# Performance work log

Measured on AMD Instinct MI355X. Metric: run time of the kernel, lower is better.

Reference implementation:

```python
import jax, jax.numpy as jnp
import numpy as np
from jax import lax

RATIO = 0.25
K = 16
EPS = 1e-5
B, N, CX, COUT, CAUX = 16, 4096, 64, 128, 32


def _fps(p, m):
    # Farthest point sampling on one cloud p:(N,3); deterministic start at index 0.
    mind = jnp.sum((p - p[0]) ** 2, axis=-1)  # (N,) min sq-dist to selected set
    def step(mind, _):
        nxt = jnp.argmax(mind)
        d = jnp.sum((p - p[nxt]) ** 2, axis=-1)
        return jnp.minimum(mind, d), nxt
    _, rest = lax.scan(step, mind, None, length=m - 1)
    return jnp.concatenate([jnp.zeros((1,), jnp.int32), rest.astype(jnp.int32)])


def setup_inputs() -> dict:
    key = jax.random.key(0)
    k1, k2, k3, k4, k5, k6 = jax.random.split(key, 6)
    P = B * N
    x = jax.random.normal(k1, (P, CX), jnp.float32)
    pos = jax.random.normal(k2, (P, 3), jnp.float32)
    batch = jnp.repeat(jnp.arange(B, dtype=jnp.int32), N)  # equal-size clouds
    aux = jax.random.normal(k3, (P, CAUX), jnp.float32)
    # MLP params: Linear(CX->COUT) + BatchNorm affine
    W = jax.random.normal(k4, (CX, COUT), jnp.float32) * (1.0 / np.sqrt(CX))
    b = jax.random.normal(k5, (COUT,), jnp.float32) * 0.02
    gamma = jnp.ones((COUT,), jnp.float32) + 0.1 * jax.random.normal(k6, (COUT,), jnp.float32)
    beta = jnp.zeros((COUT,), jnp.float32)
    return {"x": x, "pos": pos, "batch": batch, "aux": aux,
            "W": W, "b": b, "gamma": gamma, "beta": beta}


def reference(x, pos, batch, aux, W, b, gamma, beta):
    P = x.shape[0]
    nb = int(batch[-1]) + 1            # number of clouds (equal-size)
    n = P // nb
    m = int(n * RATIO)                 # clusters per cloud
    pos_b = pos.reshape(nb, n, 3)
    # --- FPS per cloud ---
    idx_local = jax.vmap(lambda p: _fps(p, m))(pos_b)                     # (B, M)
    id_clusters = (idx_local + jnp.arange(nb, dtype=jnp.int32)[:, None] * n).reshape(-1)
    centers = jnp.take_along_axis(pos_b, idx_local[..., None], axis=1)    # (B, M, 3)
    # --- kNN of all points to cluster centers, within each cloud ---
    d2 = jnp.sum((centers[:, :, None, :] - pos_b[:, None, :, :]) ** 2, axis=-1)  # (B, M, N)
    _, nb_local = lax.top_k(-d2, K)                                       # (B, M, K)
    nb_global = (nb_local + jnp.arange(nb, dtype=jnp.int32)[:, None, None] * n).reshape(-1)
    # --- MLP: Linear -> BatchNorm(batch stats, train mode) -> ReLU ---
    h = x @ W + b
    mu = jnp.mean(h, axis=0)
    var = jnp.var(h, axis=0)
    x_trans = jax.nn.relu(gamma * (h - mu) * lax.rsqrt(var + EPS) + beta)  # (P, Cout)
    # --- gather + per-cluster max / mean pooling (== scatter over knn edges) ---
    x_out = jnp.max(x_trans[nb_global].reshape(nb * m, K, -1), axis=1)     # (B*M, Cout)
    aux_out = jnp.mean(aux[nb_global].reshape(nb * m, K, -1), axis=1)      # (B*M, Caux)
    sub_pos = centers.reshape(-1, 3)
    sub_batch = batch[id_clusters]
    return x_out, sub_pos, sub_batch, aux_out, id_clusters
```

## Files before the change

### kernel.cpp

```cpp
#include <hip/hip_runtime.h>
#include <hip/hip_bf16.h>
#include <math.h>

#define NB    16
#define NPC   4096
#define MPC   1024
#define PTOT  65536
#define NCLU  16384
#define KNN_  16
#define CIN   64
#define COUT_ 128
#define CAUX_ 32

#define OFF_XOUT   0
#define OFF_SUBPOS (NCLU*COUT_)
#define OFF_SUBB   (OFF_SUBPOS + NCLU*3)
#define OFF_AUX    (OFF_SUBB + NCLU)
#define OFF_IDCL   (OFF_AUX + NCLU*CAUX_)

#define WS_H        0
#define WS_CENTERS  (PTOT*COUT_*4)
#define WS_STATS    (WS_CENTERS + NCLU*16)
#define WS_NEED     (WS_STATS + 256*4)

#define SM_LX    0
#define SM_LY    16384
#define SM_LZ    32768
#define SM_CAND  49152
#define SM_CSEL  49664
#define SM_XT    0
#define SM_WL    17408
#define SM_BS    50176
#define SM_BQ    50688
#define SM_SIZE  53760

__device__ __forceinline__ double dmax(double a, double b) { return __builtin_fmax(a, b); }
__device__ __forceinline__ double dmin(double a, double b) { return __builtin_fmin(a, b); }
__device__ __forceinline__ double pk(float d, int lo) {
  return __hiloint2double(__float_as_int(d), lo);
}
__device__ __forceinline__ int pk_lo(double k) {
  return (int)(unsigned)(__double_as_longlong(k) & 0xFFFFFFFFll);
}

template <int CTRL>
__device__ __forceinline__ double dpp64(double v) {
  long long u = __double_as_longlong(v);
  int lo = (int)(unsigned)(u & 0xFFFFFFFFll);
  int hi = (int)(unsigned)((unsigned long long)u >> 32);
  int rlo = __builtin_amdgcn_update_dpp(0, lo, CTRL, 0xf, 0xf, true);
  int rhi = __builtin_amdgcn_update_dpp(0, hi, CTRL, 0xf, 0xf, true);
  return __longlong_as_double(((long long)rhi << 32) | (long long)(unsigned)rlo);
}
#define ROR1 0x121
#define ROR2 0x122
#define ROR4 0x124
#define ROR8 0x128

__device__ __forceinline__ double rowmax16(double w) {
  w = dmax(w, dpp64<ROR1>(w));
  w = dmax(w, dpp64<ROR2>(w));
  w = dmax(w, dpp64<ROR4>(w));
  w = dmax(w, dpp64<ROR8>(w));
  return w;
}

__device__ void fps_block(char* smem, const float* __restrict__ pos,
                          float4* __restrict__ centers, float* __restrict__ out)
{
  #pragma clang fp contract(off)
  float* lx = (float*)(smem + SM_LX);
  float* ly = (float*)(smem + SM_LY);
  float* lz = (float*)(smem + SM_LZ);
  double* cand = (double*)(smem + SM_CAND);
  int*   csel = (int*)(smem + SM_CSEL);
  const int b = blockIdx.x;
  const int t = threadIdx.x;
  const float* pb = pos + (size_t)b * NPC * 3;
  const int entry  = (t >> 6) * 4 + ((t >> 4) & 3);
  const bool writer = ((t & 15) == 0);

  float px[8], py[8], pz[8], mind[8];
  int lo8[8];
  {
    const float4* src = (const float4*)(pb + t * 24);
    float4 v[6];
    #pragma unroll
    for (int i = 0; i < 6; ++i) v[i] = src[i];
    const float* f = (const float*)v;
    #pragma unroll
    for (int j = 0; j < 8; ++j) {
      px[j] = f[3*j]; py[j] = f[3*j+1]; pz[j] = f[3*j+2];
      lx[t*8+j] = px[j]; ly[t*8+j] = py[j]; lz[t*8+j] = pz[j];
      lo8[j] = 4095 - (t*8 + j);
    }
  }
  __syncthreads();
  const float x0 = lx[0], y0 = ly[0], z0 = lz[0];
  if (t == 0) csel[0] = 0;

  double bk;
  {
    double k4[4];
    #pragma unroll
    for (int jp = 0; jp < 4; ++jp) {
      const int j0 = 2*jp, j1 = 2*jp + 1;
      float dx0 = px[j0]-x0, dy0 = py[j0]-y0, dz0 = pz[j0]-z0;
      float dx1 = px[j1]-x0, dy1 = py[j1]-y0, dz1 = pz[j1]-z0;
      float d0 = (dx0*dx0 + dy0*dy0) + dz0*dz0;
      float d1 = (dx1*dx1 + dy1*dy1) + dz1*dz1;
      mind[j0] = d0; mind[j1] = d1;
      k4[jp] = dmax(pk(d0, lo8[j0]), pk(d1, lo8[j1]));
    }
    bk = dmax(dmax(k4[0], k4[1]), dmax(k4[2], k4[3]));
  }

  for (int s = 1; s < MPC; ++s) {
    double w = rowmax16(bk);
    const int ph = (s & 1) * 32;
    if (writer) cand[ph + entry] = w;
    __syncthreads();
    double2 pr = ((const double2*)(cand + ph))[t & 15];
    double w2 = rowmax16(dmax(pr.x, pr.y));
    const int sel = 4095 - pk_lo(w2);
    const float sx = lx[sel], sy = ly[sel], sz = lz[sel];
    if (t == 0) csel[s] = sel;
    double k4[4];
    #pragma unroll
    for (int jp = 0; jp < 4; ++jp) {
      const int j0 = 2*jp, j1 = 2*jp + 1;
      float dx0 = px[j0]-sx, dy0 = py[j0]-sy, dz0 = pz[j0]-sz;
      float dx1 = px[j1]-sx, dy1 = py[j1]-sy, dz1 = pz[j1]-sz;
      float d0 = (dx0*dx0 + dy0*dy0) + dz0*dz0;
      float d1 = (dx1*dx1 + dy1*dy1) + dz1*dz1;
      float m0 = fminf(mind[j0], d0), m1 = fminf(mind[j1], d1);
      mind[j0] = m0; mind[j1] = m1;
      k4[jp] = dmax(pk(m0, lo8[j0]), pk(m1, lo8[j1]));
    }
    bk = dmax(dmax(k4[0], k4[1]), dmax(k4[2], k4[3]));
  }
  __syncthreads();
  for (int c = t; c < MPC; c += 512) {
    const int il = csel[c];
    const int cl = b*MPC + c;
    const float X = lx[il], Y = ly[il], Z = lz[il];
    centers[cl] = make_float4(X, Y, Z, 0.0f);
    out[OFF_SUBPOS + cl*3 + 0] = X;
    out[OFF_SUBPOS + cl*3 + 1] = Y;
    out[OFF_SUBPOS + cl*3 + 2] = Z;
    out[OFF_SUBB + cl] = (float)b;
    out[OFF_IDCL + cl] = (float)(b*NPC + il);
  }
}

__device__ void gemm_block(char* smem, const float* __restrict__ x,
                           const float* __restrict__ W, const float* __restrict__ bias,
                           float* __restrict__ h, float* __restrict__ stats, int blk)
{
  float (*xT)[68]  = (float(*)[68])(smem + SM_XT);
  float (*Wl)[128] = (float(*)[128])(smem + SM_WL);
  float* bsum = (float*)(smem + SM_BS);
  float* bsq  = (float*)(smem + SM_BQ);
  const int t = threadIdx.x;
  const int row0 = blk * 64;
  if (t < 128) { bsum[t] = 0.0f; bsq[t] = 0.0f; }
  #pragma unroll
  for (int i = 0; i < 8; ++i) {
    const int idx = t + i*512;
    xT[idx & 63][idx >> 6] = x[(size_t)row0*64 + idx];
  }
  #pragma unroll
  for (int i = 0; i < 16; ++i) {
    const int idx = t + i*512;
    ((float*)Wl)[idx] = W[idx];
  }
  __syncthreads();
  const int tx = t & 31, ty = t >> 5;
  float acc[4][4] = {};
  #pragma unroll 8
  for (int k = 0; k < 64; ++k) {
    const float4 a  = *(const float4*)&xT[k][ty*4];
    const float4 b0 = *(const float4*)&Wl[k][tx*4];
    const float av[4] = {a.x, a.y, a.z, a.w};
    const float bw[4] = {b0.x, b0.y, b0.z, b0.w};
    #pragma unroll
    for (int i2 = 0; i2 < 4; ++i2)
      #pragma unroll
      for (int e = 0; e < 4; ++e)
        acc[i2][e] += av[i2] * bw[e];
  }
  const int c0 = tx*4;
  float bb[4];
  #pragma unroll
  for (int e = 0; e < 4; ++e) bb[e] = bias[c0+e];
  float s4[4] = {}, q4[4] = {};
  #pragma unroll
  for (int i2 = 0; i2 < 4; ++i2) {
    float vv[4];
    #pragma unroll
    for (int e = 0; e < 4; ++e) {
      float v = acc[i2][e] + bb[e];
      vv[e] = v; s4[e] += v; q4[e] += v*v;
    }
    const int r = row0 + ty*4 + i2;
    *(float4*)&h[(size_t)r*128 + c0] = make_float4(vv[0], vv[1], vv[2], vv[3]);
  }
  #pragma unroll
  for (int e = 0; e < 4; ++e) {
    atomicAdd(&bsum[c0+e], s4[e]);
    atomicAdd(&bsq[c0+e],  q4[e]);
  }
  __syncthreads();
  if (t < 128) {
    atomicAdd(&stats[t],      bsum[t]);
    atomicAdd(&stats[128+t],  bsq[t]);
  }
}

__global__ __launch_bounds__(512) void fused_fps_gemm(const float* __restrict__ pos,
                                                      float4* __restrict__ centers,
                                                      float* __restrict__ out,
                                                      const float* __restrict__ x,
                                                      const float* __restrict__ W,
                                                      const float* __restrict__ bias,
                                                      float* __restrict__ h,
                                                      float* __restrict__ stats)
{
  __shared__ __align__(16) char smem[SM_SIZE];
  if (blockIdx.x < NB) fps_block(smem, pos, centers, out);
  else                 gemm_block(smem, x, W, bias, h, stats, blockIdx.x - NB);
}

#define KBIG __hiloint2double(0x7f7fffff, 0xffffffff)
#define CD_STRIDE 17

#define KP_CD    0
#define KP_SCL   69632
#define KP_SSH   70144
#define KP_FID   70656
#define KP_SIZE  72704

__global__ __launch_bounds__(512) void knn_pool(const float* __restrict__ pos,
                                                const float4* __restrict__ centers,
                                                const float* __restrict__ h,
                                                const float* __restrict__ aux,
                                                const float* __restrict__ stats,
                                                const float* __restrict__ gamma,
                                                const float* __restrict__ beta,
                                                float* __restrict__ out)
{
  #pragma clang fp contract(off)
  __shared__ __align__(16) char sm2[KP_SIZE];
  float4* lp = (float4*)(sm2);
  double* cd = (double*)(sm2 + KP_CD);
  float*  scl = (float*)(sm2 + KP_SCL);
  float*  ssh = (float*)(sm2 + KP_SSH);
  int*    fid = (int*)(sm2 + KP_FID);
  const int vblk = ((blockIdx.x & 7) << 6) | (blockIdx.x >> 3);
  const int b   = vblk >> 5;
  const int c0  = (vblk & 31) * 32;
  const int t   = threadIdx.x;
  const int q   = t & 15;
  const int cc  = t >> 4;
  if (t < 128) {
    const float inv = 1.0f / 65536.0f;
    const float mu  = stats[t] * inv;
    const float var = stats[128+t] * inv - mu*mu;
    const float sc  = gamma[t] * rsqrtf(var + 1e-5f);
    scl[t] = sc;
    ssh[t] = beta[t] - mu*sc;
  }
  const float* pb = pos + (size_t)b * NPC * 3;
  for (int i = t; i < NPC; i += 512)
    lp[i] = make_float4(pb[3*i], pb[3*i+1], pb[3*i+2], 0.0f);
  __syncthreads();
  const float4 C = centers[b*MPC + c0 + cc];
  double L[16];
  #pragma unroll
  for (int k = 0; k < 16; ++k) L[k] = KBIG;
  for (int jj = 0; jj < NPC/16; ++jj) {
    const int j = jj*16 + q;
    const float4 p = lp[j];
    float dx = C.x - p.x, dy = C.y - p.y, dz = C.z - p.z;
    float d2 = (dx*dx + dy*dy) + dz*dz;
    double nk = pk(d2, j);
    if (nk < L[0]) {
      #pragma unroll
      for (int k = 0; k < 15; ++k) L[k] = dmin(L[k], dmax(L[k+1], nk));
      L[15] = dmin(L[15], nk);
    }
  }
  __syncthreads();
  #pragma unroll
  for (int k = 0; k < 16; ++k) cd[t*CD_STRIDE + k] = L[k];
  __syncthreads();
  if (q < 4) {
    #pragma unroll
    for (int r = 1; r <= 3; ++r) {
      const double* src = cd + (cc*16 + q + 4*r)*CD_STRIDE;
      #pragma unroll
      for (int k = 0; k < 16; ++k) {
        double nk = src[k];
        if (nk < L[0]) {
          #pragma unroll
          for (int m = 0; m < 15; ++m) L[m] = dmin(L[m], dmax(L[m+1], nk));
          L[15] = dmin(L[15], nk);
        }
      }
    }
    #pragma unroll
    for (int k = 0; k < 16; ++k) cd[t*CD_STRIDE + k] = L[k];
  }
  __syncthreads();
  if (q == 0) {
    #pragma unroll
    for (int r = 1; r <= 3; ++r) {
      const double* src = cd + (cc*16 + r)*CD_STRIDE;
      #pragma unroll
      for (int k = 0; k < 16; ++k) {
        double nk = src[k];
        if (nk < L[0]) {
          #pragma unroll
          for (int m = 0; m < 15; ++m) L[m] = dmin(L[m], dmax(L[m+1], nk));
          L[15] = dmin(L[15], nk);
        }
      }
    }
    #pragma unroll
    for (int k = 0; k < 16; ++k) fid[cc*16 + k] = b*NPC + pk_lo(L[k]);
  }
  __syncthreads();
  for (int g = 0; g < 8; ++g) {
    const int cc2 = g*4 + (t >> 7);
    const int col = t & 127;
    const int cl  = b*MPC + c0 + cc2;
    const float sc = scl[col], sh = ssh[col];
    float mv = 0.0f;
    #pragma unroll
    for (int k = 0; k < 16; ++k) {
      const float hv = h[(size_t)fid[cc2*16 + k]*128 + col];
      mv = fmaxf(mv, fmaxf(sc*hv + sh, 0.0f));
    }
    out[OFF_XOUT + (size_t)cl*128 + col] = mv;
    if (col < 32) {
      float s = 0.0f;
      #pragma unroll
      for (int k = 0; k < 16; ++k) s += aux[(size_t)fid[cc2*16 + k]*32 + col];
      out[OFF_AUX + (size_t)cl*32 + col] = s * (1.0f/16.0f);
    }
  }
}

extern "C" void kernel_launch(void* const* d_in, const int* in_sizes, int n_in,
                              void* d_out, int out_size, void* d_ws, size_t ws_size,
                              hipStream_t stream)
{
  const float* x     = (const float*)d_in[0];
  const float* pos   = (const float*)d_in[1];
  const float* aux   = (const float*)d_in[3];
  const float* W     = (const float*)d_in[4];
  const float* bias  = (const float*)d_in[5];
  const float* gamma = (const float*)d_in[6];
  const float* beta  = (const float*)d_in[7];
  float* out = (float*)d_out;
  char*  ws  = (char*)d_ws;
  if (ws_size < (size_t)WS_NEED) return;

  float*  h       = (float*)(ws + WS_H);
  float4* centers = (float4*)(ws + WS_CENTERS);
  float*  stats   = (float*)(ws + WS_STATS);

  hipMemsetAsync(stats, 0, 256*4, stream);
  hipLaunchKernelGGL(fused_fps_gemm, dim3(NB + PTOT/64), dim3(512), 0, stream,
                     pos, centers, out, x, W, bias, h, stats);
  hipLaunchKernelGGL(knn_pool, dim3(512), dim3(512), 0, stream,
                     pos, centers, h, aux, stats, gamma, beta, out);
}
```

Measured before the change: 743.4 us.

## Morton-sort points in FPS and skip distance updates via per-thread bounding boxes

Before the FPS loop, each cloud's points are binned into an 8x8x8 Morton grid using a shared-memory histogram and prefix scan, then redistributed so each thread holds 8 spatially nearby points with a tight bounding box. In each FPS iteration, a thread skips its distance update when a lower bound on the distance from its box to the new center already exceeds its current max min-distance. This is meant to cut the per-step ALU work, at the cost of extra shared memory, a setup phase and divergent branches. The skipped update is exact in intent because of the 0.99 safety factor, and tie-breaking still uses the original indices.

```diff
diff --git a/kernel.cpp b/kernel.cpp
--- a/kernel.cpp
+++ b/kernel.cpp
@@ -28,11 +28,15 @@
 #define SM_LZ    32768
 #define SM_CAND  49152
 #define SM_CSEL  49664
+#define SM_SIDX  53760
+#define SM_HIST  70144
+#define SM_SCANA 72192
+#define SM_SCANB 74240
 #define SM_XT    0
 #define SM_WL    17408
 #define SM_BS    50176
 #define SM_BQ    50688
-#define SM_SIZE  53760
+#define SM_SIZE  76288
 
 __device__ __forceinline__ double dmax(double a, double b) { return __builtin_fmax(a, b); }
 __device__ __forceinline__ double dmin(double a, double b) { return __builtin_fmin(a, b); }
@@ -52,6 +56,10 @@
   int rhi = __builtin_amdgcn_update_dpp(0, hi, CTRL, 0xf, 0xf, true);
   return __longlong_as_double(((long long)rhi << 32) | (long long)(unsigned)rlo);
 }
+template <int CTRL>
+__device__ __forceinline__ float dpp32(float x) {
+  return __int_as_float(__builtin_amdgcn_update_dpp(0, __float_as_int(x), CTRL, 0xf, 0xf, true));
+}
 #define ROR1 0x121
 #define ROR2 0x122
 #define ROR4 0x124
@@ -63,6 +71,29 @@
   w = dmax(w, dpp64<ROR4>(w));
   w = dmax(w, dpp64<ROR8>(w));
   return w;
+}
+__device__ __forceinline__ float row16maxf(float m) {
+  m = fmaxf(m, dpp32<ROR1>(m));
+  m = fmaxf(m, dpp32<ROR2>(m));
+  m = fmaxf(m, dpp32<ROR4>(m));
+  m = fmaxf(m, dpp32<ROR8>(m));
+  return m;
+}
+__device__ __forceinline__ float row16minf(float m) {
+  m = fminf(m, dpp32<ROR1>(m));
+  m = fminf(m, dpp32<ROR2>(m));
+  m = fminf(m, dpp32<ROR4>(m));
+  m = fminf(m, dpp32<ROR8>(m));
+  return m;
+}
+
+__device__ __forceinline__ int mort3(int x, int y, int z) {
+  int m = 0;
+  #pragma unroll
+  for (int bb = 0; bb < 3; ++bb)
+    m |= (((x >> bb) & 1) << (3*bb + 2)) | (((y >> bb) & 1) << (3*bb + 1)) |
+         (((z >> bb) & 1) << (3*bb));
+  return m;
 }
 
 __device__ void fps_block(char* smem, const float* __restrict__ pos,
@@ -74,14 +105,18 @@
   float* lz = (float*)(smem + SM_LZ);
   double* cand = (double*)(smem + SM_CAND);
   int*   csel = (int*)(smem + SM_CSEL);
+  int*   sidx = (int*)(smem + SM_SIDX);
+  int*   hist = (int*)(smem + SM_HIST);
+  float* bbs  = (float*)(smem + SM_HIST);
+  int*   sA   = (int*)(smem + SM_SCANA);
+  int*   sB   = (int*)(smem + SM_SCANB);
   const int b = blockIdx.x;
   const int t = threadIdx.x;
   const float* pb = pos + (size_t)b * NPC * 3;
   const int entry  = (t >> 6) * 4 + ((t >> 4) & 3);
   const bool writer = ((t & 15) == 0);
 
-  float px[8], py[8], pz[8], mind[8];
-  int lo8[8];
+  float ox[8], oy[8], oz[8];
   {
     const float4* src = (const float4*)(pb + t * 24);
     float4 v[6];
@@ -90,12 +125,77 @@
     const float* f = (const float*)v;
     #pragma unroll
     for (int j = 0; j < 8; ++j) {
-      px[j] = f[3*j]; py[j] = f[3*j+1]; pz[j] = f[3*j+2];
-      lx[t*8+j] = px[j]; ly[t*8+j] = py[j]; lz[t*8+j] = pz[j];
-      lo8[j] = 4095 - (t*8 + j);
-    }
-  }
-  __syncthreads();
+      ox[j] = f[3*j]; oy[j] = f[3*j+1]; oz[j] = f[3*j+2];
+      lx[t*8+j] = ox[j]; ly[t*8+j] = oy[j]; lz[t*8+j] = oz[j];
+    }
+  }
+  float mnx = ox[0], mxx = ox[0], mny = oy[0], mxy = oy[0], mnz = oz[0], mxz = oz[0];
+  #pragma unroll
+  for (int j = 1; j < 8; ++j) {
+    mnx = fminf(mnx, ox[j]); mxx = fmaxf(mxx, ox[j]);
+    mny = fminf(mny, oy[j]); mxy = fmaxf(mxy, oy[j]);
+    mnz = fminf(mnz, oz[j]); mxz = fmaxf(mxz, oz[j]);
+  }
+  mnx = row16minf(mnx); mxx = row16maxf(mxx);
+  mny = row16minf(mny); mxy = row16maxf(mxy);
+  mnz = row16minf(mnz); mxz = row16maxf(mxz);
+  if (writer) {
+    bbs[entry] = mnx; bbs[32+entry] = mxx; bbs[64+entry]  = mny;
+    bbs[96+entry] = mxy; bbs[128+entry] = mnz; bbs[160+entry] = mxz;
+  }
+  __syncthreads();
+  float gx0 = bbs[0], gx1 = bbs[32], gy0 = bbs[64], gy1 = bbs[96], gz0 = bbs[128], gz1 = bbs[160];
+  #pragma unroll 8
+  for (int w = 1; w < 32; ++w) {
+    gx0 = fminf(gx0, bbs[w]);     gx1 = fmaxf(gx1, bbs[32+w]);
+    gy0 = fminf(gy0, bbs[64+w]);  gy1 = fmaxf(gy1, bbs[96+w]);
+    gz0 = fminf(gz0, bbs[128+w]); gz1 = fmaxf(gz1, bbs[160+w]);
+  }
+  __syncthreads();
+  hist[t] = 0;
+  __syncthreads();
+  const float scx = 8.0f / ((gx1 - gx0) + 1e-6f);
+  const float scy = 8.0f / ((gy1 - gy0) + 1e-6f);
+  const float scz = 8.0f / ((gz1 - gz0) + 1e-6f);
+  int key[8];
+  #pragma unroll
+  for (int j = 0; j < 8; ++j) {
+    int cx = min(7, max(0, (int)((ox[j] - gx0) * scx)));
+    int cy = min(7, max(0, (int)((oy[j] - gy0) * scy)));
+    int cz = min(7, max(0, (int)((oz[j] - gz0) * scz)));
+    key[j] = mort3(cx, cy, cz);
+    atomicAdd(&hist[key[j]], 1);
+  }
+  __syncthreads();
+  const int hv = hist[t];
+  sA[t] = hv;
+  __syncthreads();
+  for (int off = 1; off < 512; off <<= 1) {
+    const int o = (t >= off) ? sA[t - off] : 0;
+    __syncthreads();
+    sA[t] += o;
+    __syncthreads();
+  }
+  sB[t] = sA[t] - hv;
+  __syncthreads();
+  #pragma unroll
+  for (int j = 0; j < 8; ++j) {
+    const int slot = atomicAdd(&sB[key[j]], 1);
+    sidx[slot] = t*8 + j;
+  }
+  __syncthreads();
+  float px[8], py[8], pz[8], mind[8];
+  int lo8[8];
+  float bxn = 1e30f, bxx = -1e30f, byn = 1e30f, byy = -1e30f, bzn = 1e30f, bzz = -1e30f;
+  #pragma unroll
+  for (int j = 0; j < 8; ++j) {
+    const int sid = sidx[t*8 + j];
+    px[j] = lx[sid]; py[j] = ly[sid]; pz[j] = lz[sid];
+    lo8[j] = 4095 - sid;
+    bxn = fminf(bxn, px[j]); bxx = fmaxf(bxx, px[j]);
+    byn = fminf(byn, py[j]); byy = fmaxf(byy, py[j]);
+    bzn = fminf(bzn, pz[j]); bzz = fmaxf(bzz, pz[j]);
+  }
   const float x0 = lx[0], y0 = ly[0], z0 = lz[0];
   if (t == 0) csel[0] = 0;
 
@@ -125,19 +225,26 @@
     const int sel = 4095 - pk_lo(w2);
     const float sx = lx[sel], sy = ly[sel], sz = lz[sel];
     if (t == 0) csel[s] = sel;
-    double k4[4];
-    #pragma unroll
-    for (int jp = 0; jp < 4; ++jp) {
-      const int j0 = 2*jp, j1 = 2*jp + 1;
-      float dx0 = px[j0]-sx, dy0 = py[j0]-sy, dz0 = pz[j0]-sz;
-      float dx1 = px[j1]-sx, dy1 = py[j1]-sy, dz1 = pz[j1]-sz;
-      float d0 = (dx0*dx0 + dy0*dy0) + dz0*dz0;
-      float d1 = (dx1*dx1 + dy1*dy1) + dz1*dz1;
-      float m0 = fminf(mind[j0], d0), m1 = fminf(mind[j1], d1);
-      mind[j0] = m0; mind[j1] = m1;
-      k4[jp] = dmax(pk(m0, lo8[j0]), pk(m1, lo8[j1]));
-    }
-    bk = dmax(dmax(k4[0], k4[1]), dmax(k4[2], k4[3]));
+    const float bkhi = __int_as_float(__double2hiint(bk));
+    const float cxd = fmaxf(fmaxf(bxn - sx, sx - bxx), 0.0f);
+    const float cyd = fmaxf(fmaxf(byn - sy, sy - byy), 0.0f);
+    const float czd = fmaxf(fmaxf(bzn - sz, sz - bzz), 0.0f);
+    const float lb = 0.99f * ((cxd*cxd + cyd*cyd) + czd*czd);
+    if (lb < bkhi) {
+      double k4[4];
+      #pragma unroll
+      for (int jp = 0; jp < 4; ++jp) {
+        const int j0 = 2*jp, j1 = 2*jp + 1;
+        float dx0 = px[j0]-sx, dy0 = py[j0]-sy, dz0 = pz[j0]-sz;
+        float dx1 = px[j1]-sx, dy1 = py[j1]-sy, dz1 = pz[j1]-sz;
+        float d0 = (dx0*dx0 + dy0*dy0) + dz0*dz0;
+        float d1 = (dx1*dx1 + dy1*dy1) + dz1*dz1;
+        float m0 = fminf(mind[j0], d0), m1 = fminf(mind[j1], d1);
+        mind[j0] = m0; mind[j1] = m1;
+        k4[jp] = dmax(pk(m0, lo8[j0]), pk(m1, lo8[j1]));
+      }
+      bk = dmax(dmax(k4[0], k4[1]), dmax(k4[2], k4[3]));
+    }
   }
   __syncthreads();
   for (int c = t; c < MPC; c += 512) {
```

Result: no change. 734.3 us, median of 2 (-1.2%).
